# Kernel optimization log

Hardware: AMD Instinct MI355X
Metric: run time of the kernel (lower is better)

The kernel has to match this reference:

```python
import jax, jax.numpy as jnp
import numpy as np

FFT_LEN = 64
BATCH = 262144  # large batch -> memory-bound; per-sample math is a tiny 64x64 DFT
PILOT_IDX = np.array([11, 25, 39, 53])


def _dft_kernels():
    # Exact replication of ComplexIFFT.__init__: cos/sin DFT matrices scaled by 1/N.
    n = np.arange(FFT_LEN).reshape(-1, 1)
    k = np.arange(FFT_LEN)
    cos_k = (np.cos(2.0 * np.pi * k * n / FFT_LEN) / FFT_LEN).astype(np.float32)
    sin_k = (np.sin(2.0 * np.pi * k * n / FFT_LEN) / FFT_LEN).astype(np.float32)
    return jnp.asarray(cos_k), jnp.asarray(sin_k)


def setup_inputs() -> dict:
    key = jax.random.key(0)
    eq_freq = jax.random.normal(key, (BATCH, 2, FFT_LEN), dtype=jnp.float32)
    cos_kernel, sin_kernel = _dft_kernels()
    return {"eq_freq": eq_freq, "cos_kernel": cos_kernel, "sin_kernel": sin_kernel}


def reference(eq_freq, cos_kernel, sin_kernel):
    # insert_pilots: set subcarriers 11/25/39/53 to (1.0 + 0.0j) on every batch row.
    idx = jnp.asarray(PILOT_IDX)
    x = eq_freq.at[:, 0, idx].set(1.0).at[:, 1, idx].set(0.0)  # (B, 2, 64)

    x_real = x[:, 0, :]  # (B, 64)
    x_imag = x[:, 1, :]

    # conv1d(1->64, kernel=64) on a length-64 signal == matmul with the 64x64 kernel:
    # out[b, n] = sum_k kernel[n, k] * x[b, k]
    rr = jnp.einsum('bk,nk->bn', x_real, cos_kernel)
    ri = jnp.einsum('bk,nk->bn', x_imag, cos_kernel)
    ir = jnp.einsum('bk,nk->bn', x_real, sin_kernel)
    ii = jnp.einsum('bk,nk->bn', x_imag, sin_kernel)

    out_real = rr - ii  # (B, 64)
    out_imag = ri + ir

    # torch: permute to (B, 64->len, 1) then cat on dim=1 -> (B, 2, 64) after squeeze semantics;
    # concretely out_real/out_imag each become (B, 1, 64) and are concatenated on dim 1.
    return jnp.stack([out_real, out_imag], axis=1)  # (B, 2, 64)
```

## Files before the change

kernel.cpp:

```cpp
#include <hip/hip_runtime.h>

typedef __attribute__((ext_vector_type(8))) short short8;
typedef __attribute__((ext_vector_type(4))) float float4v;

static __device__ inline short f2bf(float f) {
    union { float f; unsigned u; } v; v.f = f;
    unsigned u = v.u;
    u += 0x7fffu + ((u >> 16) & 1u);
    return (short)(u >> 16);
}

__global__ __launch_bounds__(256)
void build_wt(const float* __restrict__ cosk, const float* __restrict__ sink,
              short* __restrict__ wt)
{
    const int idx = blockIdx.x * 256 + threadIdx.x;
    const int n = idx >> 7, k = idx & 127;
    const int nn = n & 63, km = k & 63;
    float v;
    if (n < 64) v = (k < 64) ? cosk[n * 64 + k] : -sink[n * 64 + km];
    else        v = (k < 64) ? sink[nn * 64 + k] : cosk[nn * 64 + km];
    wt[idx] = f2bf(v);
}

typedef __attribute__((address_space(1))) const unsigned g_u32;
typedef __attribute__((address_space(3))) unsigned l_u32;
__device__ static inline void gload_lds16(void* l, const void* g) {
    __builtin_amdgcn_global_load_lds((g_u32*)g, (l_u32*)l, 16, 0, 0);
}

__global__ __launch_bounds__(256, 2)
void ofdm_idft_kernel(const float* __restrict__ eq,
                      const short* __restrict__ wt,
                      float* __restrict__ out)
{
    extern __shared__ char lds[];
    const int lane = threadIdx.x & 63;
    const int wave = threadIdx.x >> 6;
    const int m    = lane & 15;
    const int q    = lane >> 4;
    const int half = lane >> 5;
    const int pos  = lane & 31;

    char* buf0 = lds + wave * 8192;
    char* buf1 = lds + 32768 + wave * 8192;

    const int wid = blockIdx.x * 4 + wave;
    const unsigned long long PMASK =
        (1ull << 11) | (1ull << 25) | (1ull << 39) | (1ull << 53);

    auto STAGE = [&](char* B, int it) {
        const size_t tb = (size_t)(it * 2048 + wid) * 16;
        #pragma unroll
        for (int i = 0; i < 8; ++i) {
            const int r = 2 * i + half;
            const float* src = eq + (tb + r) * 128 + ((pos ^ (r & 7)) << 2);
            gload_lds16(B + i * 1024, src);
        }
    };

    STAGE(buf0, 0);

    #pragma unroll
    for (int it = 0; it < 8; ++it) {
        char* cur = (it & 1) ? buf1 : buf0;
        char* nxt = (it & 1) ? buf0 : buf1;
        if (it + 1 < 8) STAGE(nxt, it + 1);

        asm volatile("s_waitcnt vmcnt(8)" ::: "memory");
        __builtin_amdgcn_sched_barrier(0);

        short8 xfr[4];
        #pragma unroll
        for (int kk = 0; kk < 4; ++kk) {
            const int p0 = kk * 8 + q * 2;
            float4v lo = *(const float4v*)(cur + m * 512 + ((p0 ^ (m & 7)) << 4));
            float4v hi = *(const float4v*)(cur + m * 512 + (((p0 + 1) ^ (m & 7)) << 4));
            short8 f;
            #pragma unroll
            for (int j = 0; j < 8; ++j) {
                float xv = (j < 4) ? lo[j] : hi[j - 4];
                const int k = kk * 32 + q * 8 + j;
                if ((PMASK >> (k & 63)) & 1ull)
                    xv = (k < 64) ? 1.0f : 0.0f;
                f[j] = f2bf(xv);
            }
            xfr[kk] = f;
        }

        float4v acc[8];
        #pragma unroll
        for (int nt = 0; nt < 8; ++nt)
            acc[nt] = (float4v){0.f, 0.f, 0.f, 0.f};
        #pragma unroll
        for (int kk = 0; kk < 4; ++kk) {
            short8 wfr[8];
            #pragma unroll
            for (int nt = 0; nt < 8; ++nt)
                wfr[nt] = *(const short8*)(wt + (nt * 16 + m) * 128 + kk * 32 + q * 8);
            #pragma unroll
            for (int nt = 0; nt < 8; ++nt)
                acc[nt] = __builtin_amdgcn_mfma_f32_16x16x32_bf16(
                    wfr[nt], xfr[kk], acc[nt], 0, 0, 0);
        }

        #pragma unroll
        for (int nt = 0; nt < 8; ++nt) {
            const int p = nt * 4 + q;
            *(float4v*)(cur + m * 512 + ((p ^ (m & 7)) << 4)) = acc[nt];
        }

        const size_t ob = (size_t)(it * 2048 + wid) * 16 * 128;
        #pragma unroll
        for (int i = 0; i < 8; ++i) {
            const int r = 2 * i + half;
            float4v vv = *(const float4v*)(cur + r * 512 + ((pos ^ (r & 7)) << 4));
            *(float4v*)(out + ob + r * 128 + pos * 4) = vv;
        }
    }
}

extern "C" void kernel_launch(void* const* d_in, const int* in_sizes, int n_in,
                              void* d_out, int out_size, void* d_ws, size_t ws_size,
                              hipStream_t stream) {
    const float* eq   = (const float*)d_in[0];
    const float* cosk = (const float*)d_in[1];
    const float* sink = (const float*)d_in[2];
    float* out = (float*)d_out;
    short* wt  = (short*)d_ws;

    hipLaunchKernelGGL(build_wt, dim3(64), dim3(256), 0, stream, cosk, sink, wt);
    hipLaunchKernelGGL(ofdm_idft_kernel, dim3(512), dim3(256), 65536, stream,
                       eq, wt, out);
}
```

Before: 266.5 us.

## Exploit DFT block symmetry, stage weights in LDS, load inputs directly to registers

```diff
diff --git a/kernel.cpp b/kernel.cpp
--- a/kernel.cpp
+++ b/kernel.cpp
@@ -15,12 +15,9 @@
               short* __restrict__ wt)
 {
     const int idx = blockIdx.x * 256 + threadIdx.x;
-    const int n = idx >> 7, k = idx & 127;
-    const int nn = n & 63, km = k & 63;
-    float v;
-    if (n < 64) v = (k < 64) ? cosk[n * 64 + k] : -sink[n * 64 + km];
-    else        v = (k < 64) ? sink[nn * 64 + k] : cosk[nn * 64 + km];
-    wt[idx] = f2bf(v);
+    const int t = idx >> 12, n = (idx >> 6) & 63, k = idx & 63;
+    const float v = t ? sink[n * 64 + k] : cosk[n * 64 + k];
+    wt[t * 4096 + n * 64 + (((k >> 3) ^ (n & 7)) << 3) + (k & 7)] = f2bf(v);
 }
 
 typedef __attribute__((address_space(1))) const unsigned g_u32;
@@ -29,57 +26,53 @@
     __builtin_amdgcn_global_load_lds((g_u32*)g, (l_u32*)l, 16, 0, 0);
 }
 
-__global__ __launch_bounds__(256, 2)
+__global__ __launch_bounds__(256, 4)
 void ofdm_idft_kernel(const float* __restrict__ eq,
                       const short* __restrict__ wt,
                       float* __restrict__ out)
 {
-    extern __shared__ char lds[];
+    __shared__ char wlds[16384];
+    __shared__ char obuf[4][8192];
     const int lane = threadIdx.x & 63;
     const int wave = threadIdx.x >> 6;
     const int m    = lane & 15;
     const int q    = lane >> 4;
     const int half = lane >> 5;
     const int pos  = lane & 31;
+    const int wid  = blockIdx.x * 4 + wave;
 
-    char* buf0 = lds + wave * 8192;
-    char* buf1 = lds + 32768 + wave * 8192;
+    #pragma unroll
+    for (int i = 0; i < 4; ++i)
+        gload_lds16(wlds + wave * 4096 + i * 1024,
+                    (const char*)wt + wave * 4096 + i * 1024 + lane * 16);
+    asm volatile("s_waitcnt vmcnt(0)" ::: "memory");
+    __syncthreads();
 
-    const int wid = blockIdx.x * 4 + wave;
     const unsigned long long PMASK =
         (1ull << 11) | (1ull << 25) | (1ull << 39) | (1ull << 53);
-
-    auto STAGE = [&](char* B, int it) {
-        const size_t tb = (size_t)(it * 2048 + wid) * 16;
-        #pragma unroll
-        for (int i = 0; i < 8; ++i) {
-            const int r = 2 * i + half;
-            const float* src = eq + (tb + r) * 128 + ((pos ^ (r & 7)) << 2);
-            gload_lds16(B + i * 1024, src);
-        }
-    };
-
-    STAGE(buf0, 0);
+    const char* Ct = wlds;
+    const char* St = wlds + 8192;
+    char* ob = obuf[wave];
 
     #pragma unroll
-    for (int it = 0; it < 8; ++it) {
-        char* cur = (it & 1) ? buf1 : buf0;
-        char* nxt = (it & 1) ? buf0 : buf1;
-        if (it + 1 < 8) STAGE(nxt, it + 1);
+    for (int it = 0; it < 4; ++it) {
+        const size_t tb = ((size_t)wid * 4 + it) * 16;
 
-        asm volatile("s_waitcnt vmcnt(8)" ::: "memory");
-        __builtin_amdgcn_sched_barrier(0);
+        float4v x[8];
+        const float* a = eq + (tb + m) * 128 + q * 8;
+        #pragma unroll
+        for (int kk = 0; kk < 4; ++kk) {
+            x[kk * 2 + 0] = *(const float4v*)(a + kk * 32);
+            x[kk * 2 + 1] = *(const float4v*)(a + kk * 32 + 4);
+        }
 
         short8 xfr[4];
         #pragma unroll
         for (int kk = 0; kk < 4; ++kk) {
-            const int p0 = kk * 8 + q * 2;
-            float4v lo = *(const float4v*)(cur + m * 512 + ((p0 ^ (m & 7)) << 4));
-            float4v hi = *(const float4v*)(cur + m * 512 + (((p0 + 1) ^ (m & 7)) << 4));
             short8 f;
             #pragma unroll
             for (int j = 0; j < 8; ++j) {
-                float xv = (j < 4) ? lo[j] : hi[j - 4];
+                float xv = (j < 4) ? x[kk * 2][j] : x[kk * 2 + 1][j - 4];
                 const int k = kk * 32 + q * 8 + j;
                 if ((PMASK >> (k & 63)) & 1ull)
                     xv = (k < 64) ? 1.0f : 0.0f;
@@ -87,35 +80,45 @@
             }
             xfr[kk] = f;
         }
+        short8 nx2, nx3;
+        #pragma unroll
+        for (int j = 0; j < 8; ++j) {
+            nx2[j] = xfr[2][j] ^ (short)0x8000;
+            nx3[j] = xfr[3][j] ^ (short)0x8000;
+        }
 
         float4v acc[8];
         #pragma unroll
         for (int nt = 0; nt < 8; ++nt)
             acc[nt] = (float4v){0.f, 0.f, 0.f, 0.f};
         #pragma unroll
-        for (int kk = 0; kk < 4; ++kk) {
-            short8 wfr[8];
-            #pragma unroll
-            for (int nt = 0; nt < 8; ++nt)
-                wfr[nt] = *(const short8*)(wt + (nt * 16 + m) * 128 + kk * 32 + q * 8);
-            #pragma unroll
-            for (int nt = 0; nt < 8; ++nt)
-                acc[nt] = __builtin_amdgcn_mfma_f32_16x16x32_bf16(
-                    wfr[nt], xfr[kk], acc[nt], 0, 0, 0);
+        for (int t = 0; t < 4; ++t) {
+            const int row = (t * 16 + m) * 128;
+            short8 Cf0 = *(const short8*)(Ct + row + (((q    ) ^ (m & 7)) << 4));
+            short8 Cf1 = *(const short8*)(Ct + row + (((q + 4) ^ (m & 7)) << 4));
+            short8 Sf0 = *(const short8*)(St + row + (((q    ) ^ (m & 7)) << 4));
+            short8 Sf1 = *(const short8*)(St + row + (((q + 4) ^ (m & 7)) << 4));
+            acc[t] = __builtin_amdgcn_mfma_f32_16x16x32_bf16(Cf0, xfr[0], acc[t], 0, 0, 0);
+            acc[t] = __builtin_amdgcn_mfma_f32_16x16x32_bf16(Cf1, xfr[1], acc[t], 0, 0, 0);
+            acc[t] = __builtin_amdgcn_mfma_f32_16x16x32_bf16(Sf0, nx2,    acc[t], 0, 0, 0);
+            acc[t] = __builtin_amdgcn_mfma_f32_16x16x32_bf16(Sf1, nx3,    acc[t], 0, 0, 0);
+            acc[t + 4] = __builtin_amdgcn_mfma_f32_16x16x32_bf16(Sf0, xfr[0], acc[t + 4], 0, 0, 0);
+            acc[t + 4] = __builtin_amdgcn_mfma_f32_16x16x32_bf16(Sf1, xfr[1], acc[t + 4], 0, 0, 0);
+            acc[t + 4] = __builtin_amdgcn_mfma_f32_16x16x32_bf16(Cf0, xfr[2], acc[t + 4], 0, 0, 0);
+            acc[t + 4] = __builtin_amdgcn_mfma_f32_16x16x32_bf16(Cf1, xfr[3], acc[t + 4], 0, 0, 0);
         }
 
         #pragma unroll
         for (int nt = 0; nt < 8; ++nt) {
             const int p = nt * 4 + q;
-            *(float4v*)(cur + m * 512 + ((p ^ (m & 7)) << 4)) = acc[nt];
+            *(float4v*)(ob + m * 512 + ((p ^ (m & 7)) << 4)) = acc[nt];
         }
 
-        const size_t ob = (size_t)(it * 2048 + wid) * 16 * 128;
         #pragma unroll
         for (int i = 0; i < 8; ++i) {
             const int r = 2 * i + half;
-            float4v vv = *(const float4v*)(cur + r * 512 + ((pos ^ (r & 7)) << 4));
-            *(float4v*)(out + ob + r * 128 + pos * 4) = vv;
+            float4v vv = *(const float4v*)(ob + r * 512 + ((pos ^ (r & 7)) << 4));
+            *(float4v*)(out + (tb + r) * 128 + pos * 4) = vv;
         }
     }
 }
@@ -129,7 +132,7 @@
     float* out = (float*)d_out;
     short* wt  = (short*)d_ws;
 
-    hipLaunchKernelGGL(build_wt, dim3(64), dim3(256), 0, stream, cosk, sink, wt);
-    hipLaunchKernelGGL(ofdm_idft_kernel, dim3(512), dim3(256), 65536, stream,
+    hipLaunchKernelGGL(build_wt, dim3(32), dim3(256), 0, stream, cosk, sink, wt);
+    hipLaunchKernelGGL(ofdm_idft_kernel, dim3(1024), dim3(256), 0, stream,
                        eq, wt, out);
 }
```

Result: faster. 241.6 us (-9.3%).
